# Performance work log

Measured on AMD Instinct MI355X. Metric: run time of the kernel, lower is better.

## Reference

```python
import jax, jax.numpy as jnp
import numpy as np

K = 20
EPS = 1e-5
SLOPE = 0.2


def get_graph_feature(x, k):
    # x: [B, N, C]. DGCNN: knn on negative squared distance, gather, concat(nbr-ctr, ctr).
    sq = jnp.sum(x * x, axis=-1)                              # [B,N]
    inner = jnp.einsum('bnc,bmc->bnm', x, x)                  # [B,N,N]
    pdist = 2.0 * inner - sq[:, :, None] - sq[:, None, :]     # -||xi-xj||^2
    idx = jax.lax.top_k(pdist, k)[1]                          # [B,N,k] nearest (incl. self)
    b = jnp.arange(x.shape[0])[:, None, None]
    nbr = x[b, idx]                                           # [B,N,k,C]
    ctr = jnp.broadcast_to(x[:, :, None, :], nbr.shape)
    return jnp.concatenate([nbr - ctr, ctr], axis=-1)         # [B,N,k,2C]


def edgeconv(x, W, gamma, beta, mean, var):
    # 1x1 Conv2d (no bias) + BatchNorm2d (eval mode) + LeakyReLU(0.2) + max over k
    feat = get_graph_feature(x, K)                            # [B,N,k,2C]
    y = jnp.einsum('bnkc,oc->bnko', feat, W)                  # [B,N,k,O]
    y = (y - mean) * (gamma / jnp.sqrt(var + EPS)) + beta
    y = jnp.where(y >= 0, y, SLOPE * y)
    return jnp.max(y, axis=2)                                 # [B,N,O]


def dgcnn_pass(x, p1, p2, p3):
    x = edgeconv(x, *p1)
    x = edgeconv(x, *p2)
    x = edgeconv(x, *p3)
    return x                                                  # [B,N,F3]


def attention(emb, W_att):
    # SimGNN attention pooling (batched)
    ctx = jnp.tanh(jnp.mean(jnp.einsum('bnf,fg->bng', emb, W_att), axis=1))  # [B,F]
    s = jax.nn.sigmoid(jnp.einsum('bnf,bf->bn', emb, ctx))                   # [B,N]
    return jnp.einsum('bnf,bn->bf', emb, s)                                  # [B,F]


def tensor_network(e1, e2, W_t, W_block, bias):
    scoring = jnp.einsum('bf,fgt,bg->bt', e1, W_t, e2)        # [B,T]
    comb = jnp.concatenate([e1, e2], axis=1)                  # [B,2F]
    block = jnp.einsum('tf,bf->bt', W_block, comb)            # [B,T]
    return jax.nn.relu(scoring + block + bias)


def setup_inputs() -> dict:
    key = jax.random.key(0)
    ks = jax.random.split(key, 16)
    B, N, C = 8, 2048, 12
    F = 64
    T = 16
    d = {}
    d['graph1'] = jax.random.normal(ks[0], (B, N, C), jnp.float32)
    d['graph2'] = jax.random.normal(ks[1], (B, N, C), jnp.float32)
    d['W1'] = jax.random.normal(ks[2], (F, 2 * C), jnp.float32) * 0.1
    d['g1'] = jax.random.uniform(ks[3], (F,), jnp.float32, 0.5, 1.5)
    d['b1'] = jax.random.normal(ks[4], (F,), jnp.float32) * 0.1
    d['m1'] = jnp.zeros((F,), jnp.float32)
    d['v1'] = jnp.ones((F,), jnp.float32)
    d['W2'] = jax.random.normal(ks[5], (F, 2 * F), jnp.float32) * 0.1
    d['g2'] = jax.random.uniform(ks[6], (F,), jnp.float32, 0.5, 1.5)
    d['b2'] = jax.random.normal(ks[7], (F,), jnp.float32) * 0.1
    d['m2'] = jnp.zeros((F,), jnp.float32)
    d['v2'] = jnp.ones((F,), jnp.float32)
    d['W3'] = jax.random.normal(ks[8], (F, 2 * F), jnp.float32) * 0.1
    d['g3'] = jax.random.uniform(ks[9], (F,), jnp.float32, 0.5, 1.5)
    d['b3'] = jax.random.normal(ks[10], (F,), jnp.float32) * 0.1
    d['m3'] = jnp.zeros((F,), jnp.float32)
    d['v3'] = jnp.ones((F,), jnp.float32)
    d['W_att'] = jax.random.normal(ks[11], (F, F), jnp.float32) * 0.1
    d['W_tensor'] = jax.random.normal(ks[12], (F, F, T), jnp.float32) * 0.05
    d['W_block'] = jax.random.normal(ks[13], (T, 2 * F), jnp.float32) * 0.1
    d['bias_tn'] = jax.random.normal(ks[14], (T,), jnp.float32) * 0.1
    return d


def reference(graph1, graph2, W1, g1, b1, m1, v1, W2, g2, b2, m2, v2,
              W3, g3, b3, m3, v3, W_att, W_tensor, W_block, bias_tn):
    p1 = (W1, g1, b1, m1, v1)
    p2 = (W2, g2, b2, m2, v2)
    p3 = (W3, g3, b3, m3, v3)
    emb1 = dgcnn_pass(graph1, p1, p2, p3)   # [B,N,F]
    emb2 = dgcnn_pass(graph2, p1, p2, p3)
    e1 = attention(emb1, W_att)             # [B,F]
    e2 = attention(emb2, W_att)
    return tensor_network(e1, e2, W_tensor, W_block, bias_tn)  # [B,T]
```

## Files before the change

kernel.cpp:

```cpp
#include <hip/hip_runtime.h>
#include <hip/hip_bf16.h>
#include <float.h>

#define DEV __device__ __forceinline__

using f32x4 = __attribute__((ext_vector_type(4))) float;
using f4v   = __attribute__((ext_vector_type(4))) float;
using bfrag = __attribute__((ext_vector_type(8))) short;
using hfrag = __attribute__((ext_vector_type(8))) _Float16;
using us8   = __attribute__((ext_vector_type(8))) unsigned short;

DEV unsigned short f2bf(float f) {
  unsigned u = __builtin_bit_cast(unsigned, f);
  u += 0x7FFFu + ((u >> 16) & 1u);
  return (unsigned short)(u >> 16);
}
DEV float bf2f(unsigned short h) {
  unsigned u = ((unsigned)h) << 16;
  return __builtin_bit_cast(float, u);
}
DEV f32x4 mfma_bf(bfrag a, bfrag b, f32x4 c) {
  return __builtin_amdgcn_mfma_f32_16x16x32_bf16(a, b, c, 0, 0, 0);
}
DEV f32x4 mfma_h(hfrag a, hfrag b, f32x4 c) {
  return __builtin_amdgcn_mfma_f32_16x16x32_f16(a, b, c, 0, 0, 0);
}
DEV float readlane_f(float v, int l) {
  return __builtin_bit_cast(float,
      __builtin_amdgcn_readlane(__builtin_bit_cast(int, v), l));
}

template<int RB>
DEV unsigned swz(int row, int colb) {
  return (unsigned)(row * RB) +
         (((unsigned)colb) ^ (((unsigned)(row << 4)) & (unsigned)(RB - 1)));
}
template<int RB>
DEV bfrag ldfragB(const unsigned short* base, int row, int kcol) {
  return *(const bfrag*)((const char*)base + swz<RB>(row, kcol * 2));
}
template<int RB>
DEV hfrag ldfragH(const _Float16* base, int row, int kcol) {
  return *(const hfrag*)((const char*)base + swz<RB>(row, kcol * 2));
}

template<int C, int C32>
DEV void stageHL(const float* __restrict__ src, unsigned short* H,
                 unsigned short* L, int tid) {
  constexpr int RB  = C32 * 2;
  constexpr int CH8 = C32 / 8;
  if (tid < 64 * CH8) {
    const int row = tid / CH8, cb = (tid % CH8) * 8;
    float f[8];
    if constexpr (C % 8 == 0) {
      *(f4v*)(f + 0) = *(const f4v*)(src + row * C + cb);
      *(f4v*)(f + 4) = *(const f4v*)(src + row * C + cb + 4);
    } else {
#pragma unroll
      for (int e = 0; e < 8; ++e) {
        const int c = cb + e;
        f[e] = (c < C) ? src[row * C + c] : 0.f;
      }
    }
    us8 hv, lv;
#pragma unroll
    for (int e = 0; e < 8; ++e) {
      const unsigned short hs = f2bf(f[e]);
      hv[e] = hs;
      lv[e] = f2bf(f[e] - bf2f(hs));
    }
    const unsigned off = swz<RB>(row, cb * 2);
    *(us8*)((char*)H + off) = hv;
    *(us8*)((char*)L + off) = lv;
  }
}

DEV void bitonic64(float& v, int& ix, int lane) {
#pragma unroll
  for (int k = 2; k <= 64; k <<= 1) {
#pragma unroll
    for (int j = k >> 1; j > 0; j >>= 1) {
      const float ov = __shfl_xor(v, j);
      const int   oi = __shfl_xor(ix, j);
      const bool up = (lane & k) != 0;
      const bool iWin = (v > ov) || (v == ov && ix < oi);
      const bool keepBetter = (((lane & j) == 0) != up);
      if (iWin != keepBetter) { v = ov; ix = oi; }
    }
  }
}

template<int C>
DEV const float* xbase(const float* xA, const float* xB, int b) {
  return (b < 8) ? xA + (size_t)b * 2048 * C
                 : xB + (size_t)(b - 8) * 2048 * C;
}

template<int C>
__global__ __launch_bounds__(256)
void sq_kernel(const float* __restrict__ xA, const float* __restrict__ xB,
               float* __restrict__ sq) {
  const int i = blockIdx.x * 256 + threadIdx.x;
  const int b = i >> 11, n = i & 2047;
  const float* r = xbase<C>(xA, xB, b) + (size_t)n * C;
  float s = 0.f;
#pragma unroll
  for (int c = 0; c < C; c += 4) {
    f4v v = *(const f4v*)(r + c);
    s += v[0] * v[0] + v[1] * v[1] + v[2] * v[2] + v[3] * v[3];
  }
  sq[i] = s;
}

template<int C, int C32>
__global__ __launch_bounds__(1024)
void knn_kernel(const float* __restrict__ xA, const float* __restrict__ xB,
                const float* __restrict__ sqg, int* __restrict__ idx_out) {
  constexpr int N = 2048, TI = 64, TJ = 64, TK = 20, NT = N / TJ;
  constexpr int RB = C32 * 2;
  const int b    = blockIdx.x >> 5;
  const int i0   = (blockIdx.x & 31) * TI;
  const int tid  = threadIdx.x;
  const int lane = tid & 63;
  const int w    = tid >> 6;
  const int ri   = w >> 2;
  const int ci   = w & 3;

  __shared__ unsigned short XiH[TI * C32], XiL[TI * C32];
  __shared__ unsigned short XjH[TJ * C32], XjL[TJ * C32];
  __shared__ float S[TI][TJ + 4];
  __shared__ float sqT[TJ];

  const float* xb = xbase<C>(xA, xB, b);
  const int m15 = lane & 15;
  const int kb8 = (lane >> 4) * 8;

  stageHL<C, C32>(xb + (size_t)i0 * C, XiH, XiL, tid);

  float tv[4], t20[4]; int tix[4];
#pragma unroll
  for (int d = 0; d < 4; ++d) { tv[d] = -FLT_MAX; tix[d] = 0; t20[d] = -FLT_MAX; }

  for (int jt = 0; jt < NT; ++jt) {
    const int j0 = jt * TJ;
    stageHL<C, C32>(xb + (size_t)j0 * C, XjH, XjL, tid);
    if (tid < TJ) sqT[tid] = sqg[b * N + j0 + tid];
    __syncthreads();

    f32x4 acc = {0, 0, 0, 0};
#pragma unroll
    for (int ks = 0; ks < C32 / 32; ++ks) {
      const int kc = ks * 32 + kb8;
      const bfrag ah = ldfragB<RB>(XiH, 16 * ri + m15, kc);
      const bfrag al = ldfragB<RB>(XiL, 16 * ri + m15, kc);
      const bfrag bh = ldfragB<RB>(XjH, 16 * ci + m15, kc);
      const bfrag bl = ldfragB<RB>(XjL, 16 * ci + m15, kc);
      acc = mfma_bf(ah, bh, acc);
      acc = mfma_bf(ah, bl, acc);
      acc = mfma_bf(al, bh, acc);
    }
#pragma unroll
    for (int r = 0; r < 4; ++r)
      S[16 * ri + (lane >> 4) * 4 + r][16 * ci + m15] = acc[r];
    const float sqv = sqT[lane];
    __syncthreads();

#pragma unroll
    for (int d = 0; d < 4; ++d) {
      const float sc = 2.f * S[4 * w + d][lane] - sqv;
      if (jt == 0) {
        float v = sc; int ixv = lane;
        bitonic64(v, ixv, lane);
        tv[d]  = (lane < TK) ? v : -FLT_MAX;
        tix[d] = (lane < TK) ? ixv : 0;
        t20[d] = readlane_f(tv[d], TK - 1);
      } else {
        unsigned long long mm = __ballot(sc > t20[d]);
        if (mm) {
          while (mm) {
            const int src = __ffsll(mm) - 1;
            mm &= mm - 1;
            const float cv = readlane_f(sc, src);
            const int   ci2 = j0 + src;
            const float pv_ = __shfl_up(tv[d], 1);
            const int   pi_ = __shfl_up(tix[d], 1);
            const unsigned long long g =
                __ballot(tv[d] > cv || (tv[d] == cv && tix[d] < ci2));
            const int p = __popcll(g);
            float nv = (lane == p) ? cv  : ((lane > p) ? pv_ : tv[d]);
            int   ni = (lane == p) ? ci2 : ((lane > p) ? pi_ : tix[d]);
            tv[d]  = (lane >= TK) ? -FLT_MAX : nv;
            tix[d] = (lane >= TK) ? 0 : ni;
          }
          t20[d] = readlane_f(tv[d], TK - 1);
        }
      }
    }
  }
  if (lane < TK) {
#pragma unroll
    for (int d = 0; d < 4; ++d) {
      const int i = i0 + 4 * w + d;
      idx_out[((size_t)b * N + i) * TK + lane] = tix[d];
    }
  }
}

template<int C, int C32>
__global__ __launch_bounds__(256)
void conv_kernel(const float* __restrict__ xA, const float* __restrict__ xB,
                 const int* __restrict__ idxg,
                 const float* __restrict__ W, const float* __restrict__ gam,
                 const float* __restrict__ bet, const float* __restrict__ mea,
                 const float* __restrict__ var, float* __restrict__ y) {
  constexpr int N = 2048, TK = 20, O = 64;
  constexpr int RB = C32 * 2;
  constexpr int CH8 = C32 / 8;
  const int b    = blockIdx.x >> 7;
  const int n0   = (blockIdx.x & 127) * 16;
  const int tid  = threadIdx.x;
  const int lane = tid & 63;
  const int w    = tid >> 6;

  __shared__ float    ctrF[16][C];
  __shared__ _Float16 A1[320 * C32];
  __shared__ _Float16 CtrB[16 * C32];
  __shared__ _Float16 WdT[O * C32];
  __shared__ _Float16 WcT[O * C32];

  const float* xb = xbase<C>(xA, xB, b);

  for (int i = tid; i < 16 * C; i += 256)
    ctrF[i / C][i % C] = xb[(size_t)(n0 + i / C) * C + (i % C)];

  for (int i = tid; i < O * CH8; i += 256) {
    const int o = i / CH8, ch = (i % CH8) * 8;
    hfrag hd, hc;
#pragma unroll
    for (int e = 0; e < 8; ++e) {
      const int c = ch + e;
      hd[e] = (c < C) ? (_Float16)W[o * 2 * C + c]     : (_Float16)0.f;
      hc[e] = (c < C) ? (_Float16)W[o * 2 * C + C + c] : (_Float16)0.f;
    }
    const unsigned off = swz<RB>(o, ch * 2);
    *(hfrag*)((char*)WdT + off) = hd;
    *(hfrag*)((char*)WcT + off) = hc;
  }
  __syncthreads();

  for (int i = tid; i < 16 * CH8; i += 256) {
    const int row = i / CH8, ch = (i % CH8) * 8;
    hfrag hv;
#pragma unroll
    for (int e = 0; e < 8; ++e) {
      const int c = ch + e;
      hv[e] = (c < C) ? (_Float16)ctrF[row][c] : (_Float16)0.f;
    }
    *(hfrag*)((char*)CtrB + swz<RB>(row, ch * 2)) = hv;
  }

  for (int r = tid; r < 16 * TK; r += 256) {
    const int n = r & 15, k = r >> 4;
    int j = idxg[((size_t)b * N + n0 + n) * TK + k];
    j &= (N - 1);
    const float* xj = xb + (size_t)j * C;
#pragma unroll
    for (int ch = 0; ch < C32; ch += 8) {
      float f[8];
#pragma unroll
      for (int q = 0; q < 8; q += 4) {
        const int c = ch + q;
        if (c + 3 < C) {
          *(f4v*)(f + q) = *(const f4v*)(xj + c);
        } else {
#pragma unroll
          for (int e = 0; e < 4; ++e) f[q + e] = (c + e < C) ? xj[c + e] : 0.f;
        }
      }
      hfrag hv;
#pragma unroll
      for (int e = 0; e < 8; ++e) {
        const int c = ch + e;
        const float d = (c < C) ? (f[e] - ctrF[n][c]) : 0.f;
        hv[e] = (_Float16)d;
      }
      *(hfrag*)((char*)A1 + swz<RB>(r, ch * 2)) = hv;
    }
  }
  __syncthreads();

  const int m15 = lane & 15;
  const int kb8 = (lane >> 4) * 8;
  hfrag bd[C32 / 32], bc[C32 / 32];
#pragma unroll
  for (int ks = 0; ks < C32 / 32; ++ks) {
    bd[ks] = ldfragH<RB>(WdT, 16 * w + m15, ks * 32 + kb8);
    bc[ks] = ldfragH<RB>(WcT, 16 * w + m15, ks * 32 + kb8);
  }
  f32x4 base = {0, 0, 0, 0};
#pragma unroll
  for (int ks = 0; ks < C32 / 32; ++ks)
    base = mfma_h(ldfragH<RB>(CtrB, m15, ks * 32 + kb8), bc[ks], base);

  f32x4 mx = {-FLT_MAX, -FLT_MAX, -FLT_MAX, -FLT_MAX};
#pragma unroll
  for (int k = 0; k < TK; ++k) {
    f32x4 a = {0, 0, 0, 0};
#pragma unroll
    for (int ks = 0; ks < C32 / 32; ++ks)
      a = mfma_h(ldfragH<RB>(A1, 16 * k + m15, ks * 32 + kb8), bd[ks], a);
#pragma unroll
    for (int r = 0; r < 4; ++r) mx[r] = fmaxf(mx[r], a[r] + base[r]);
  }

  const int o = 16 * w + m15;
  const float scv = gam[o] / sqrtf(var[o] + 1e-5f);
  const float shv = bet[o] - mea[o] * scv;
#pragma unroll
  for (int r = 0; r < 4; ++r) {
    const int n = (lane >> 4) * 4 + r;
    float v = scv * mx[r] + shv;
    v = (v >= 0.f) ? v : 0.2f * v;
    y[((size_t)b * N + n0 + n) * O + o] = v;
  }
}

__global__ __launch_bounds__(256)
void att_mean_kernel(const float* __restrict__ emb, float* __restrict__ msum) {
  constexpr int N = 2048, F = 64;
  const int b    = blockIdx.x >> 4;
  const int slab = blockIdx.x & 15;
  const int tid  = threadIdx.x;
  const int f = tid & 63, p = tid >> 6;
  __shared__ float part[4][F];
  float acc = 0.f;
  const float* e = emb + ((size_t)b * N + slab * 128) * F;
  for (int n = p; n < 128; n += 4) acc += e[(size_t)n * F + f];
  part[p][f] = acc;
  __syncthreads();
  if (tid < F)
    atomicAdd(&msum[b * F + tid],
              part[0][tid] + part[1][tid] + part[2][tid] + part[3][tid]);
}

__global__ __launch_bounds__(64)
void att_ctx_kernel(const float* __restrict__ msum, const float* __restrict__ Watt,
                    float* __restrict__ ctx) {
  constexpr int N = 2048, F = 64;
  const int b = blockIdx.x, tid = threadIdx.x;
  __shared__ float m[F];
  m[tid] = msum[b * F + tid] * (1.f / N);
  __syncthreads();
  float a = 0.f;
  for (int ff = 0; ff < F; ++ff) a += m[ff] * Watt[ff * F + tid];
  ctx[b * F + tid] = tanhf(a);
}

__global__ __launch_bounds__(256)
void att2_kernel(const float* __restrict__ emb, const float* __restrict__ ctx,
                 float* __restrict__ eout) {
  constexpr int N = 2048, F = 64;
  const int b   = blockIdx.x >> 3;
  const int c0  = (blockIdx.x & 7) * 256;
  const int tid = threadIdx.x, lane = tid & 63, w = tid >> 6;
  const float cv = ctx[b * F + lane];
  float acc = 0.f;
  const float* e = emb + (size_t)b * N * F;
  for (int n = c0 + w * 64; n < c0 + (w + 1) * 64; ++n) {
    const float v = e[(size_t)n * F + lane];
    float d = v * cv;
#pragma unroll
    for (int off = 1; off < 64; off <<= 1) d += __shfl_xor(d, off);
    const float s = 1.f / (1.f + expf(-d));
    acc += v * s;
  }
  atomicAdd(&eout[b * F + lane], acc);
}

__global__ __launch_bounds__(256)
void tn_kernel(const float* __restrict__ ep,
               const float* __restrict__ Wt, const float* __restrict__ Wb,
               const float* __restrict__ bias, float* __restrict__ out) {
  constexpr int F = 64, T = 16;
  const int b = blockIdx.x, tid = threadIdx.x;
  __shared__ float s1[F], s2[F];
  __shared__ float part[T][17];
  if (tid < F) { s1[tid] = ep[b * F + tid]; s2[tid] = ep[(b + 8) * F + tid]; }
  __syncthreads();
  const int t = tid >> 4, sub = tid & 15;
  float a = 0.f;
  for (int f = sub * 4; f < sub * 4 + 4; ++f) {
    float inner = 0.f;
    for (int g = 0; g < F; ++g) inner += Wt[((f * F) + g) * T + t] * s2[g];
    a += s1[f] * inner;
  }
  part[t][sub] = a;
  __syncthreads();
  if (tid < T) {
    float v = 0.f;
    for (int q = 0; q < 16; ++q) v += part[tid][q];
    for (int f = 0; f < F; ++f)
      v += Wb[tid * 2 * F + f] * s1[f] + Wb[tid * 2 * F + F + f] * s2[f];
    v += bias[tid];
    out[b * T + tid] = fmaxf(v, 0.f);
  }
}

extern "C" void kernel_launch(void* const* d_in, const int* in_sizes, int n_in,
                              void* d_out, int out_size, void* d_ws, size_t ws_size,
                              hipStream_t stream) {
  const float* x1  = (const float*)d_in[0];
  const float* x2  = (const float*)d_in[1];
  const float* W1  = (const float*)d_in[2];
  const float* g1  = (const float*)d_in[3];
  const float* b1  = (const float*)d_in[4];
  const float* m1  = (const float*)d_in[5];
  const float* v1  = (const float*)d_in[6];
  const float* W2  = (const float*)d_in[7];
  const float* g2  = (const float*)d_in[8];
  const float* b2  = (const float*)d_in[9];
  const float* m2  = (const float*)d_in[10];
  const float* v2  = (const float*)d_in[11];
  const float* W3  = (const float*)d_in[12];
  const float* g3  = (const float*)d_in[13];
  const float* b3  = (const float*)d_in[14];
  const float* m3  = (const float*)d_in[15];
  const float* v3  = (const float*)d_in[16];
  const float* Wat = (const float*)d_in[17];
  const float* Wt  = (const float*)d_in[18];
  const float* Wb  = (const float*)d_in[19];
  const float* bs  = (const float*)d_in[20];
  float* out = (float*)d_out;

  constexpr size_t NF = (size_t)16 * 2048 * 64;
  float* bufA = (float*)d_ws;
  float* bufB = bufA + NF;
  float* sqb  = bufB + NF;
  int*   idxb = (int*)(sqb + 16 * 2048);
  float* msum = (float*)(idxb + (size_t)16 * 2048 * 20);
  float* epool= msum + 16 * 64;
  float* ctx  = epool + 16 * 64;

  const float* bA8 = bufA + (size_t)8 * 2048 * 64;
  const float* bB8 = bufB + (size_t)8 * 2048 * 64;

  sq_kernel<12><<<128, 256, 0, stream>>>(x1, x2, sqb);
  knn_kernel<12, 32><<<512, 1024, 0, stream>>>(x1, x2, sqb, idxb);
  conv_kernel<12, 32><<<2048, 256, 0, stream>>>(x1, x2, idxb, W1, g1, b1, m1, v1, bufA);

  sq_kernel<64><<<128, 256, 0, stream>>>(bufA, bA8, sqb);
  knn_kernel<64, 64><<<512, 1024, 0, stream>>>(bufA, bA8, sqb, idxb);
  conv_kernel<64, 64><<<2048, 256, 0, stream>>>(bufA, bA8, idxb, W2, g2, b2, m2, v2, bufB);

  sq_kernel<64><<<128, 256, 0, stream>>>(bufB, bB8, sqb);
  knn_kernel<64, 64><<<512, 1024, 0, stream>>>(bufB, bB8, sqb, idxb);
  conv_kernel<64, 64><<<2048, 256, 0, stream>>>(bufB, bB8, idxb, W3, g3, b3, m3, v3, bufA);

  hipMemsetAsync(msum, 0, 2 * 16 * 64 * sizeof(float), stream);
  att_mean_kernel<<<256, 256, 0, stream>>>(bufA, msum);
  att_ctx_kernel<<<16, 64, 0, stream>>>(msum, Wat, ctx);
  att2_kernel<<<128, 256, 0, stream>>>(bufA, ctx, epool);
  tn_kernel<<<8, 256, 0, stream>>>(epool, Wt, Wb, bs, out);
}
```

Before: 1.001 ms.

## Precompute swizzled bf16 hi/lo tiles once and shrink KNN row tile

A new cvt_kernel converts the point features into bf16 high/low split pairs once per layer. It writes them to a workspace buffer already in the swizzled shared-memory tile layout. The KNN kernel then stages tiles with plain 16-byte copies instead of every block redoing the fp32 load and split for all column tiles. The KNN row tile also drops from 64 to 32 rows with 512-thread blocks and twice as many blocks. The cost is an extra launch and workspace traffic per layer, plus more blocks that each reread the column tiles.

```diff
diff --git a/kernel.cpp b/kernel.cpp
--- a/kernel.cpp
+++ b/kernel.cpp
@@ -44,34 +44,15 @@
   return *(const hfrag*)((const char*)base + swz<RB>(row, kcol * 2));
 }
 
-template<int C, int C32>
-DEV void stageHL(const float* __restrict__ src, unsigned short* H,
-                 unsigned short* L, int tid) {
-  constexpr int RB  = C32 * 2;
-  constexpr int CH8 = C32 / 8;
-  if (tid < 64 * CH8) {
-    const int row = tid / CH8, cb = (tid % CH8) * 8;
-    float f[8];
-    if constexpr (C % 8 == 0) {
-      *(f4v*)(f + 0) = *(const f4v*)(src + row * C + cb);
-      *(f4v*)(f + 4) = *(const f4v*)(src + row * C + cb + 4);
-    } else {
-#pragma unroll
-      for (int e = 0; e < 8; ++e) {
-        const int c = cb + e;
-        f[e] = (c < C) ? src[row * C + c] : 0.f;
-      }
-    }
-    us8 hv, lv;
-#pragma unroll
-    for (int e = 0; e < 8; ++e) {
-      const unsigned short hs = f2bf(f[e]);
-      hv[e] = hs;
-      lv[e] = f2bf(f[e] - bf2f(hs));
-    }
-    const unsigned off = swz<RB>(row, cb * 2);
-    *(us8*)((char*)H + off) = hv;
-    *(us8*)((char*)L + off) = lv;
+template<int BYTES>
+DEV void cpyN(const char* __restrict__ g, char* __restrict__ l, int tid) {
+  if constexpr (BYTES >= 8192) {
+#pragma unroll
+    for (int o = 0; o < BYTES; o += 8192)
+      *(us8*)(l + o + tid * 16) = *(const us8*)(g + o + tid * 16);
+  } else {
+    const int o = tid * 16;
+    if (o < BYTES) *(us8*)(l + o) = *(const us8*)(g + o);
   }
 }
 
@@ -113,48 +94,90 @@
 }
 
 template<int C, int C32>
-__global__ __launch_bounds__(1024)
-void knn_kernel(const float* __restrict__ xA, const float* __restrict__ xB,
-                const float* __restrict__ sqg, int* __restrict__ idx_out) {
-  constexpr int N = 2048, TI = 64, TJ = 64, TK = 20, NT = N / TJ;
-  constexpr int RB = C32 * 2;
-  const int b    = blockIdx.x >> 5;
-  const int i0   = (blockIdx.x & 31) * TI;
+__global__ __launch_bounds__(256)
+void cvt_kernel(const float* __restrict__ xA, const float* __restrict__ xB,
+                char* __restrict__ xhl) {
+  constexpr int CH8 = C32 / 8, RB = C32 * 2, HB = 64 * RB;
+  const int idx = blockIdx.x * 256 + threadIdx.x;
+  const int chunk = idx & (CH8 - 1);
+  const int rg = idx / CH8;
+  const int b = rg >> 11, n = rg & 2047;
+  const float* src = xbase<C>(xA, xB, b) + (size_t)n * C;
+  const int cb = chunk * 8;
+  float f[8];
+  if constexpr (C % 8 == 0) {
+    *(f4v*)(f + 0) = *(const f4v*)(src + cb);
+    *(f4v*)(f + 4) = *(const f4v*)(src + cb + 4);
+  } else {
+#pragma unroll
+    for (int e = 0; e < 8; ++e) {
+      const int c = cb + e;
+      f[e] = (c < C) ? src[c] : 0.f;
+    }
+  }
+  us8 hv, lv;
+#pragma unroll
+  for (int e = 0; e < 8; ++e) {
+    const unsigned short hs = f2bf(f[e]);
+    hv[e] = hs;
+    lv[e] = f2bf(f[e] - bf2f(hs));
+  }
+  char* dst = xhl + (size_t)(b * 32 + (n >> 6)) * 2 * HB;
+  const unsigned off = swz<RB>(n & 63, cb * 2);
+  *(us8*)(dst + off) = hv;
+  *(us8*)(dst + HB + off) = lv;
+}
+
+template<int C32>
+__global__ __launch_bounds__(512)
+void knn_kernel(const char* __restrict__ xhl, const float* __restrict__ sqg,
+                int* __restrict__ idx_out) {
+  constexpr int N = 2048, TI = 32, TJ = 64, TK = 20, NT = N / TJ;
+  constexpr int RB = C32 * 2, HB = 64 * RB, TILEB = 2 * HB, HBi = TI * RB;
+  const int b    = blockIdx.x >> 6;
+  const int it   = blockIdx.x & 63;
+  const int i0   = it * TI;
   const int tid  = threadIdx.x;
   const int lane = tid & 63;
   const int w    = tid >> 6;
   const int ri   = w >> 2;
   const int ci   = w & 3;
 
-  __shared__ unsigned short XiH[TI * C32], XiL[TI * C32];
-  __shared__ unsigned short XjH[TJ * C32], XjL[TJ * C32];
+  __shared__ us8 XiV[2 * HBi / 16];
+  __shared__ us8 XjV[TILEB / 16];
   __shared__ float S[TI][TJ + 4];
   __shared__ float sqT[TJ];
 
-  const float* xb = xbase<C>(xA, xB, b);
-  const int m15 = lane & 15;
-  const int kb8 = (lane >> 4) * 8;
-
-  stageHL<C, C32>(xb + (size_t)i0 * C, XiH, XiL, tid);
+  char* XiC = (char*)XiV;
+  char* XjC = (char*)XjV;
+  const unsigned short* XiHp = (const unsigned short*)XiC;
+  const unsigned short* XiLp = (const unsigned short*)(XiC + HBi);
+  const unsigned short* XjHp = (const unsigned short*)XjC;
+  const unsigned short* XjLp = (const unsigned short*)(XjC + HB);
+  const int m15 = lane & 15, kb8 = (lane >> 4) * 8;
+
+  const char* gti = xhl + (size_t)(b * 32 + (i0 >> 6)) * TILEB + (i0 & 63) * RB;
+  cpyN<HBi>(gti, XiC, tid);
+  cpyN<HBi>(gti + HB, XiC + HBi, tid);
 
   float tv[4], t20[4]; int tix[4];
 #pragma unroll
   for (int d = 0; d < 4; ++d) { tv[d] = -FLT_MAX; tix[d] = 0; t20[d] = -FLT_MAX; }
 
   for (int jt = 0; jt < NT; ++jt) {
-    const int j0 = jt * TJ;
-    stageHL<C, C32>(xb + (size_t)j0 * C, XjH, XjL, tid);
-    if (tid < TJ) sqT[tid] = sqg[b * N + j0 + tid];
+    const char* gtj = xhl + (size_t)(b * 32 + jt) * TILEB;
+    cpyN<TILEB>(gtj, XjC, tid);
+    if (tid < TJ) sqT[tid] = sqg[b * N + jt * TJ + tid];
     __syncthreads();
 
     f32x4 acc = {0, 0, 0, 0};
 #pragma unroll
     for (int ks = 0; ks < C32 / 32; ++ks) {
       const int kc = ks * 32 + kb8;
-      const bfrag ah = ldfragB<RB>(XiH, 16 * ri + m15, kc);
-      const bfrag al = ldfragB<RB>(XiL, 16 * ri + m15, kc);
-      const bfrag bh = ldfragB<RB>(XjH, 16 * ci + m15, kc);
-      const bfrag bl = ldfragB<RB>(XjL, 16 * ci + m15, kc);
+      const bfrag ah = ldfragB<RB>(XiHp, 16 * ri + m15, kc);
+      const bfrag al = ldfragB<RB>(XiLp, 16 * ri + m15, kc);
+      const bfrag bh = ldfragB<RB>(XjHp, 16 * ci + m15, kc);
+      const bfrag bl = ldfragB<RB>(XjLp, 16 * ci + m15, kc);
       acc = mfma_bf(ah, bh, acc);
       acc = mfma_bf(ah, bl, acc);
       acc = mfma_bf(al, bh, acc);
@@ -165,6 +188,7 @@
     const float sqv = sqT[lane];
     __syncthreads();
 
+    const int j0 = jt * TJ;
 #pragma unroll
     for (int d = 0; d < 4; ++d) {
       const float sc = 2.f * S[4 * w + d][lane] - sqv;
@@ -433,11 +457,13 @@
   float* out = (float*)d_out;
 
   constexpr size_t NF = (size_t)16 * 2048 * 64;
+  constexpr size_t XHLB = (size_t)16 * 32 * 16384;
   float* bufA = (float*)d_ws;
   float* bufB = bufA + NF;
   float* sqb  = bufB + NF;
   int*   idxb = (int*)(sqb + 16 * 2048);
-  float* msum = (float*)(idxb + (size_t)16 * 2048 * 20);
+  char*  xhl  = (char*)(idxb + (size_t)16 * 2048 * 20);
+  float* msum = (float*)(xhl + XHLB);
   float* epool= msum + 16 * 64;
   float* ctx  = epool + 16 * 64;
 
@@ -445,15 +471,18 @@
   const float* bB8 = bufB + (size_t)8 * 2048 * 64;
 
   sq_kernel<12><<<128, 256, 0, stream>>>(x1, x2, sqb);
-  knn_kernel<12, 32><<<512, 1024, 0, stream>>>(x1, x2, sqb, idxb);
+  cvt_kernel<12, 32><<<512, 256, 0, stream>>>(x1, x2, xhl);
+  knn_kernel<32><<<1024, 512, 0, stream>>>(xhl, sqb, idxb);
   conv_kernel<12, 32><<<2048, 256, 0, stream>>>(x1, x2, idxb, W1, g1, b1, m1, v1, bufA);
 
   sq_kernel<64><<<128, 256, 0, stream>>>(bufA, bA8, sqb);
-  knn_kernel<64, 64><<<512, 1024, 0, stream>>>(bufA, bA8, sqb, idxb);
+  cvt_kernel<64, 64><<<1024, 256, 0, stream>>>(bufA, bA8, xhl);
+  knn_kernel<64><<<1024, 512, 0, stream>>>(xhl, sqb, idxb);
   conv_kernel<64, 64><<<2048, 256, 0, stream>>>(bufA, bA8, idxb, W2, g2, b2, m2, v2, bufB);
 
   sq_kernel<64><<<128, 256, 0, stream>>>(bufB, bB8, sqb);
-  knn_kernel<64, 64><<<512, 1024, 0, stream>>>(bufB, bB8, sqb, idxb);
+  cvt_kernel<64, 64><<<1024, 256, 0, stream>>>(bufB, bB8, xhl);
+  knn_kernel<64><<<1024, 512, 0, stream>>>(xhl, sqb, idxb);
   conv_kernel<64, 64><<<2048, 256, 0, stream>>>(bufB, bB8, idxb, W3, g3, b3, m3, v3, bufA);
 
   hipMemsetAsync(msum, 0, 2 * 16 * 64 * sizeof(float), stream);
```

Result: faster. 937.4 us (-6.4%).
